# Kernel tuning notes

Hardware: AMD Instinct MI355X
Metric: run time of the kernel (lower is better)

Reference implementation:

```python
import jax, jax.numpy as jnp
import numpy as np

B, NQ, NC1, NC2 = 2, 1024, 1024, 1024
QD = CD1 = CD2 = 1024
H, DH = 8, 64
INNER = H * DH          # 512
VD = 1024               # v_dim, split across heads -> 128 per head
VDH = VD // H


def setup_inputs() -> dict:
    key = jax.random.key(0)
    ks = jax.random.split(key, 18)
    f = lambda k, shape: jax.random.normal(k, shape, jnp.float32) * 0.02
    return {
        "x": f(ks[0], (B, NQ, QD)),
        "context": f(ks[1], (B, NC1, CD1)),
        "context2": f(ks[2], (B, NC2, CD2)),
        "mask1": jax.random.uniform(ks[3], (B, NQ, NC1)) > 0.1,
        "mask2": jax.random.uniform(ks[4], (B, NQ, NC2)) > 0.1,
        "Wq": f(ks[5], (QD, INNER)),  "bq": f(ks[6], (INNER,)),
        "Wk1": f(ks[7], (CD1, INNER)), "bk1": f(ks[8], (INNER,)),
        "Wv1": f(ks[9], (CD1, VD)),    "bv1": f(ks[10], (VD,)),
        "Wk2": f(ks[11], (CD2, INNER)), "bk2": f(ks[12], (INNER,)),
        "Wv2": f(ks[13], (CD2, VD)),    "bv2": f(ks[14], (VD,)),
        "Wo": f(ks[15], (VD, VD)),      "bo": f(ks[16], (VD,)),
    }


def _split_heads(t, d):
    # b n (h d) -> b h n d
    b, n, _ = t.shape
    return t.reshape(b, n, H, d).transpose(0, 2, 1, 3)


def reference(x, context, context2, mask1, mask2,
              Wq, bq, Wk1, bk1, Wv1, bv1, Wk2, bk2, Wv2, bv2, Wo, bo):
    scale = DH ** -0.5
    q = x @ Wq + bq
    k = jnp.concatenate([context @ Wk1 + bk1, context2 @ Wk2 + bk2], axis=1)
    v = jnp.concatenate([context @ Wv1 + bv1, context2 @ Wv2 + bv2], axis=1)

    qh = _split_heads(q, DH)   # [B,H,NQ,DH]
    kh = _split_heads(k, DH)   # [B,H,NC1+NC2,DH]
    vh = _split_heads(v, VDH)  # [B,H,NC1+NC2,VDH]

    sim = jnp.einsum('bhid,bhjd->bhij', qh, kh) * scale  # [B,H,NQ,J]
    mask = jnp.concatenate([mask1, mask2], axis=2)[:, None, :, :]  # [B,1,NQ,J]
    max_neg = -jnp.finfo(sim.dtype).max
    sim = jnp.where(mask, sim, max_neg)

    attn = jax.nn.softmax(sim, axis=-1)
    out = jnp.einsum('bhij,bhjd->bhid', attn, vh)          # [B,H,NQ,VDH]
    out = out.transpose(0, 2, 1, 3).reshape(B, NQ, VD)     # b n (h d)
    return out @ Wo + bo
```

## Files before the change

kernel.cpp:

```cpp
#include <hip/hip_runtime.h>
#include <math.h>

typedef short bf16x8 __attribute__((ext_vector_type(8)));
typedef float f32x4  __attribute__((ext_vector_type(4)));

__device__ __forceinline__ unsigned short f2bf(float f) {
    unsigned int u = __builtin_bit_cast(unsigned int, f);
    u += 0x7FFFu + ((u >> 16) & 1u);
    return (unsigned short)(u >> 16);
}

__device__ __forceinline__ void gld16(const unsigned short* g, unsigned short* l) {
    __builtin_amdgcn_global_load_lds(
        (const __attribute__((address_space(1))) void*)g,
        (__attribute__((address_space(3))) void*)l, 16, 0, 0);
}

__global__ __launch_bounds__(256) void cast3(
    const float* __restrict__ a0, const float* __restrict__ a1, const float* __restrict__ a2,
    unsigned short* __restrict__ o0, unsigned short* __restrict__ o1, unsigned short* __restrict__ o2)
{
    const int z = blockIdx.z;
    const float* a = z == 0 ? a0 : (z == 1 ? a1 : a2);
    unsigned short* o = z == 0 ? o0 : (z == 1 ? o1 : o2);
    size_t i = ((size_t)blockIdx.x * 256 + threadIdx.x) * 8;
    float4 x0 = *(const float4*)&a[i];
    float4 x1 = *(const float4*)&a[i + 4];
    uint4 pk;
    pk.x = (unsigned)f2bf(x0.x) | ((unsigned)f2bf(x0.y) << 16);
    pk.y = (unsigned)f2bf(x0.z) | ((unsigned)f2bf(x0.w) << 16);
    pk.z = (unsigned)f2bf(x1.x) | ((unsigned)f2bf(x1.y) << 16);
    pk.w = (unsigned)f2bf(x1.z) | ((unsigned)f2bf(x1.w) << 16);
    *(uint4*)&o[i] = pk;
}

__global__ __launch_bounds__(256) void cast_t3(
    const float* __restrict__ W0, const float* __restrict__ W1, const float* __restrict__ W2,
    unsigned short* __restrict__ T0, unsigned short* __restrict__ T1, unsigned short* __restrict__ T2,
    int K, int N)
{
    __shared__ float T[64][65];
    const int z = blockIdx.z;
    const float* W = z == 0 ? W0 : (z == 1 ? W1 : W2);
    unsigned short* O = z == 0 ? T0 : (z == 1 ? T1 : T2);
    const int n0 = blockIdx.x << 6, k0 = blockIdx.y << 6;
    const int t = threadIdx.x;
    #pragma unroll
    for (int i = 0; i < 4; i++) {
        int vi = t + (i << 8);
        int r = vi >> 4, c4 = (vi & 15) << 2;
        *(float4*)&T[r][c4] = *(const float4*)&W[(size_t)(k0 + r) * N + n0 + c4];
    }
    __syncthreads();
    #pragma unroll
    for (int i = 0; i < 4; i++) {
        int vi = t + (i << 8);
        int n = vi >> 4, k4 = (vi & 15) << 2;
        uint2 pk;
        pk.x = (unsigned)f2bf(T[k4 + 0][n]) | ((unsigned)f2bf(T[k4 + 1][n]) << 16);
        pk.y = (unsigned)f2bf(T[k4 + 2][n]) | ((unsigned)f2bf(T[k4 + 3][n]) << 16);
        *(uint2*)&O[(size_t)(n0 + n) * K + k0 + k4] = pk;
    }
}

__global__ __launch_bounds__(256) void pack_mask(
    const int* __restrict__ mask1, const int* __restrict__ mask2,
    unsigned long long* __restrict__ mpk)
{
    int wid = (blockIdx.x << 2) + (threadIdx.x >> 6);
    int lane = threadIdx.x & 63;
    const int* m1 = mask1 + ((size_t)wid << 10);
    const int* m2 = mask2 + ((size_t)wid << 10);
    unsigned long long* o = mpk + ((size_t)wid << 5);
    #pragma unroll
    for (int win = 0; win < 16; win++) {
        unsigned long long bal = __ballot(m1[(win << 6) + lane] != 0);
        if (lane == 0) o[win] = bal;
    }
    #pragma unroll
    for (int win = 0; win < 16; win++) {
        unsigned long long bal = __ballot(m2[(win << 6) + lane] != 0);
        if (lane == 0) o[16 + win] = bal;
    }
}

template<int NT>
__device__ __forceinline__ void gemm_core(
    const unsigned short* __restrict__ A,
    const unsigned short* __restrict__ Wt,
    int K, int gm0, int gn0,
    unsigned short (*As)[32], unsigned short (*Bs)[32],
    f32x4 (&acc)[4][NT / 32])
{
    constexpr int NS = NT / 32;
    const int t = threadIdx.x;
    const int lane = t & 63, w = t >> 6;
    const int wm = (w & 1) << 6, wn = (w >> 1) * (NT / 2);
    const int l15 = lane & 15, quad = lane >> 4;

    for (int k0 = 0; k0 < K; k0 += 32) {
        __syncthreads();
        #pragma unroll
        for (int i = 0; i < 2; i++) {
            int r0 = (i << 6) + (w << 4);
            int ra = r0 + (lane >> 2);
            int kc = (lane & 3) << 3;
            gld16(&A[(size_t)(gm0 + ra) * K + k0 + kc], &As[r0][0] + ((size_t)lane << 3));
        }
        #pragma unroll
        for (int i = 0; i < NT / 64; i++) {
            int r0 = (i << 6) + (w << 4);
            int ra = r0 + (lane >> 2);
            int kc = (lane & 3) << 3;
            gld16(&Wt[(size_t)(gn0 + ra) * K + k0 + kc], &Bs[r0][0] + ((size_t)lane << 3));
        }
        __syncthreads();
        bf16x8 af[4], bg[NS];
        #pragma unroll
        for (int i = 0; i < 4; i++)
            af[i] = *(const bf16x8*)&As[wm + (i << 4) + l15][quad << 3];
        #pragma unroll
        for (int j = 0; j < NS; j++)
            bg[j] = *(const bf16x8*)&Bs[wn + (j << 4) + l15][quad << 3];
        #pragma unroll
        for (int i = 0; i < 4; i++)
            #pragma unroll
            for (int j = 0; j < NS; j++)
                acc[i][j] = __builtin_amdgcn_mfma_f32_16x16x32_bf16(af[i], bg[j], acc[i][j], 0, 0, 0);
    }
}

__global__ __launch_bounds__(256) void proj_all(
    const unsigned short* __restrict__ xb, const unsigned short* __restrict__ c1b,
    const unsigned short* __restrict__ c2b,
    const unsigned short* __restrict__ Wqt, const unsigned short* __restrict__ Wk1t,
    const unsigned short* __restrict__ Wk2t, const unsigned short* __restrict__ Wv1t,
    const unsigned short* __restrict__ Wv2t,
    const float* __restrict__ bq, const float* __restrict__ bk1, const float* __restrict__ bk2,
    const float* __restrict__ bv1, const float* __restrict__ bv2,
    unsigned short* __restrict__ qbuf, unsigned short* __restrict__ kbuf,
    unsigned short* __restrict__ vbT)
{
    __shared__ unsigned short As[128][32];
    __shared__ unsigned short Bs[128][32];
    const int bid = blockIdx.x;
    int z, bx, by;
    if (bid < 192) { z = bid >> 6; int l = bid & 63; by = l >> 2; bx = l & 3; }
    else { int l = bid - 192; z = 3 + (l >> 7); l &= 127; by = l >> 3; bx = l & 7; }
    const unsigned short* A  = (z == 0) ? xb : (z == 1 || z == 3) ? c1b : c2b;
    const unsigned short* Wt = (z == 0) ? Wqt : (z == 1) ? Wk1t : (z == 2) ? Wk2t
                             : (z == 3) ? Wv1t : Wv2t;
    const float* bias = (z == 0) ? bq : (z == 1) ? bk1 : (z == 2) ? bk2
                      : (z == 3) ? bv1 : bv2;
    const int gm0 = by << 7, gn0 = bx << 7;

    f32x4 acc[4][4];
    #pragma unroll
    for (int i = 0; i < 4; i++)
        #pragma unroll
        for (int j = 0; j < 4; j++) acc[i][j] = (f32x4){0.f, 0.f, 0.f, 0.f};

    gemm_core<128>(A, Wt, 1024, gm0, gn0, As, Bs, acc);

    const int lane = threadIdx.x & 63, w = threadIdx.x >> 6;
    const int wm = (w & 1) << 6, wn = (w >> 1) << 6;
    const int l15 = lane & 15, quad = lane >> 4;
    float bb[4];
    #pragma unroll
    for (int j = 0; j < 4; j++) bb[j] = bias[gn0 + wn + (j << 4) + l15];

    if (z < 3) {
        unsigned short* out = (z == 0) ? qbuf : kbuf;
        const int obs = (z == 0) ? 1024 : 2048;
        const int off = (z == 2) ? 1024 : 0;
        #pragma unroll
        for (int i = 0; i < 4; i++) {
            int mb = gm0 + wm + (i << 4) + (quad << 2);
            #pragma unroll
            for (int p = 0; p < 4; p++) {
                int m = mb + p;
                int orow = ((m >> 10) * obs) + off + (m & 1023);
                #pragma unroll
                for (int j = 0; j < 4; j++)
                    out[(size_t)orow * 512 + gn0 + wn + (j << 4) + l15] = f2bf(acc[i][j][p] + bb[j]);
            }
        }
    } else {
        const int off = (z == 3) ? 0 : 1024;
        #pragma unroll
        for (int i = 0; i < 4; i++) {
            int mb = gm0 + wm + (i << 4) + (quad << 2);
            int b = mb >> 10;
            int jj = (mb & 1023) + off;
            #pragma unroll
            for (int j = 0; j < 4; j++) {
                int n = gn0 + wn + (j << 4) + l15;
                unsigned long long pk = 0;
                #pragma unroll
                for (int p = 0; p < 4; p++)
                    pk |= (unsigned long long)f2bf(acc[i][j][p] + bb[j]) << (16 * p);
                *(unsigned long long*)&vbT[((size_t)b * 1024 + n) * 2048 + jj] = pk;
            }
        }
    }
}

__global__ __launch_bounds__(256) void gemm_out(
    const unsigned short* __restrict__ abuf, const unsigned short* __restrict__ Wot,
    const float* __restrict__ bo, float* __restrict__ out)
{
    __shared__ unsigned short As[128][32];
    __shared__ unsigned short Bs[64][32];
    const int gm0 = blockIdx.y << 7, gn0 = blockIdx.x << 6;

    f32x4 acc[4][2];
    #pragma unroll
    for (int i = 0; i < 4; i++)
        #pragma unroll
        for (int j = 0; j < 2; j++) acc[i][j] = (f32x4){0.f, 0.f, 0.f, 0.f};

    gemm_core<64>(abuf, Wot, 1024, gm0, gn0, As, Bs, acc);

    const int lane = threadIdx.x & 63, w = threadIdx.x >> 6;
    const int wm = (w & 1) << 6, wn = (w >> 1) << 5;
    const int l15 = lane & 15, quad = lane >> 4;
    float bb[2];
    #pragma unroll
    for (int j = 0; j < 2; j++) bb[j] = bo[gn0 + wn + (j << 4) + l15];
    #pragma unroll
    for (int i = 0; i < 4; i++) {
        int mb = gm0 + wm + (i << 4) + (quad << 2);
        #pragma unroll
        for (int p = 0; p < 4; p++)
            #pragma unroll
            for (int j = 0; j < 2; j++)
                out[(size_t)(mb + p) * 1024 + gn0 + wn + (j << 4) + l15] = acc[i][j][p] + bb[j];
    }
}

__global__ __launch_bounds__(256) void attn_mfma(
    const unsigned short* __restrict__ qbuf, const unsigned short* __restrict__ kbuf,
    const unsigned short* __restrict__ vbT, const unsigned long long* __restrict__ mpk,
    float* __restrict__ Opart, float* __restrict__ ml)
{
    __shared__ unsigned short Ks[128][64];
    __shared__ unsigned short VsT[128][128];
    __shared__ unsigned short Ps[64][132];

    const int t = threadIdx.x;
    const int bid = blockIdx.x;
    const int hs = bid >> 8, r = bid & 255;
    const int h = r & 7, qt = (r >> 3) & 15, b = r >> 7;
    const int q0 = qt << 6;
    const int lane = t & 63, w = t >> 6, l15 = lane & 15, quad = lane >> 4;

    const unsigned short* qrow = qbuf + (((size_t)(b << 10) + q0 + (w << 4) + l15) << 9) + (h << 6);
    const bf16x8 aq0 = *(const bf16x8*)&qrow[quad << 3];
    const bf16x8 aq1 = *(const bf16x8*)&qrow[32 + (quad << 3)];

    f32x4 acc[8];
    #pragma unroll
    for (int ct = 0; ct < 8; ct++) acc[ct] = (f32x4){0.f, 0.f, 0.f, 0.f};
    float m_l = -3.0e38f, l_l = 0.f;

    const size_t kbase = (size_t)b << 20;
    const size_t vbase = ((size_t)((b << 10) + (h << 7))) << 11;
    const unsigned long long* mrow = mpk + (((size_t)(b << 10) + q0 + (w << 4) + l15) << 5);

    for (int jt = 0; jt < 8; jt++) {
        const int j0 = (hs << 10) + (jt << 7);
        __syncthreads();
        #pragma unroll
        for (int i = 0; i < 4; i++) {
            int vi = t + (i << 8);
            int row = vi >> 3, c = vi & 7;
            *(uint4*)&Ks[row][(c ^ (row & 7)) << 3] =
                *(const uint4*)&kbuf[kbase + ((size_t)(j0 + row) << 9) + (h << 6) + (c << 3)];
        }
        #pragma unroll
        for (int i = 0; i < 8; i++) {
            int vi = t + (i << 8);
            int f = vi >> 4, c = vi & 15;
            int sc = (c & 8) | ((c & 7) ^ (f & 7));
            *(uint4*)&VsT[f][sc << 3] =
                *(const uint4*)&vbT[vbase + ((size_t)f << 11) + j0 + (c << 3)];
        }
        __syncthreads();

        f32x4 s[8];
        #pragma unroll
        for (int n = 0; n < 8; n++) {
            int rowk = (n << 4) + l15;
            bf16x8 bk0 = *(const bf16x8*)&Ks[rowk][(quad ^ (l15 & 7)) << 3];
            bf16x8 bk1 = *(const bf16x8*)&Ks[rowk][((quad | 4) ^ (l15 & 7)) << 3];
            s[n] = (f32x4){0.f, 0.f, 0.f, 0.f};
            s[n] = __builtin_amdgcn_mfma_f32_16x16x32_bf16(bk0, aq0, s[n], 0, 0, 0);
            s[n] = __builtin_amdgcn_mfma_f32_16x16x32_bf16(bk1, aq1, s[n], 0, 0, 0);
        }

        const int wbase = j0 >> 6;
        const unsigned long long w0 = mrow[wbase], w1 = mrow[wbase + 1];
        #pragma unroll
        for (int n = 0; n < 8; n++) {
            unsigned long long wd = (n < 4) ? w0 : w1;
            int bit0 = ((n & 3) << 4) + (quad << 2);
            #pragma unroll
            for (int p = 0; p < 4; p++) {
                float sv = s[n][p] * 0.125f;
                s[n][p] = ((wd >> (bit0 + p)) & 1ull) ? sv : -3.0e38f;
            }
        }

        float mt = s[0][0];
        #pragma unroll
        for (int n = 0; n < 8; n++)
            #pragma unroll
            for (int p = 0; p < 4; p++) mt = fmaxf(mt, s[n][p]);
        mt = fmaxf(mt, __shfl_xor(mt, 16, 64));
        mt = fmaxf(mt, __shfl_xor(mt, 32, 64));
        float mn = fmaxf(m_l, mt);
        float ls = 0.f;
        #pragma unroll
        for (int n = 0; n < 8; n++) {
            float e0 = __expf(s[n][0] - mn), e1 = __expf(s[n][1] - mn);
            float e2 = __expf(s[n][2] - mn), e3 = __expf(s[n][3] - mn);
            ls += (e0 + e1) + (e2 + e3);
            unsigned long long pk = (unsigned long long)f2bf(e0)
                | ((unsigned long long)f2bf(e1) << 16)
                | ((unsigned long long)f2bf(e2) << 32)
                | ((unsigned long long)f2bf(e3) << 48);
            *(unsigned long long*)&Ps[(w << 4) + l15][(n << 4) + (quad << 2)] = pk;
        }
        ls += __shfl_xor(ls, 16, 64);
        ls += __shfl_xor(ls, 32, 64);
        float al = __expf(m_l - mn);
        l_l = l_l * al + ls;
        m_l = mn;

        float ar[4];
        #pragma unroll
        for (int p = 0; p < 4; p++)
            ar[p] = __shfl(al, (lane & 48) | ((quad << 2) + p), 64);
        #pragma unroll
        for (int ct = 0; ct < 8; ct++)
            #pragma unroll
            for (int p = 0; p < 4; p++) acc[ct][p] *= ar[p];

        bf16x8 ap[4];
        #pragma unroll
        for (int win = 0; win < 4; win++)
            ap[win] = *(const bf16x8*)&Ps[(w << 4) + l15][(win << 5) + (quad << 3)];
        #pragma unroll
        for (int ct = 0; ct < 8; ct++) {
            int fv = (ct << 4) + l15;
            #pragma unroll
            for (int win = 0; win < 4; win++) {
                int c = (win << 2) + quad;
                int sc = (c & 8) | ((c & 7) ^ (l15 & 7));
                bf16x8 bv = *(const bf16x8*)&VsT[fv][sc << 3];
                acc[ct] = __builtin_amdgcn_mfma_f32_16x16x32_bf16(ap[win], bv, acc[ct], 0, 0, 0);
            }
        }
    }

    #pragma unroll
    for (int p = 0; p < 4; p++) {
        int q = q0 + (w << 4) + (quad << 2) + p;
        size_t idx = (size_t)(hs << 14) + (b << 13) + (h << 10) + q;
        #pragma unroll
        for (int ct = 0; ct < 8; ct++)
            Opart[(idx << 7) + (ct << 4) + l15] = acc[ct][p];
    }
    if (quad == 0) {
        int q = q0 + (w << 4) + l15;
        size_t idx = (size_t)(hs << 14) + (b << 13) + (h << 10) + q;
        ml[(idx << 1) + 0] = m_l;
        ml[(idx << 1) + 1] = l_l;
    }
}

__global__ __launch_bounds__(256) void attn_combine(
    const float* __restrict__ Opart, const float* __restrict__ ml,
    unsigned short* __restrict__ abuf)
{
    int id = (blockIdx.x << 8) + threadIdx.x;
    int bhq = id >> 5, c4 = (id & 31) << 2;
    float2 ml0 = ((const float2*)ml)[bhq];
    float2 ml1 = ((const float2*)ml)[16384 + bhq];
    float M = fmaxf(ml0.x, ml1.x);
    float a0 = __expf(ml0.x - M), a1 = __expf(ml1.x - M);
    float inv = 1.0f / (ml0.y * a0 + ml1.y * a1);
    float4 o0 = *(const float4*)&Opart[((size_t)bhq << 7) + c4];
    float4 o1 = *(const float4*)&Opart[((size_t)(16384 + bhq) << 7) + c4];
    int b = bhq >> 13, hh = (bhq >> 10) & 7, q = bhq & 1023;
    float r0 = (o0.x * a0 + o1.x * a1) * inv;
    float r1 = (o0.y * a0 + o1.y * a1) * inv;
    float r2 = (o0.z * a0 + o1.z * a1) * inv;
    float r3 = (o0.w * a0 + o1.w * a1) * inv;
    unsigned long long pk = (unsigned long long)f2bf(r0)
        | ((unsigned long long)f2bf(r1) << 16)
        | ((unsigned long long)f2bf(r2) << 32)
        | ((unsigned long long)f2bf(r3) << 48);
    *(unsigned long long*)&abuf[((size_t)((b << 10) + q) << 10) + (hh << 7) + c4] = pk;
}

extern "C" void kernel_launch(void* const* d_in, const int* in_sizes, int n_in,
                              void* d_out, int out_size, void* d_ws, size_t ws_size,
                              hipStream_t stream)
{
    const float* x        = (const float*)d_in[0];
    const float* context  = (const float*)d_in[1];
    const float* context2 = (const float*)d_in[2];
    const int*   mask1    = (const int*)d_in[3];
    const int*   mask2    = (const int*)d_in[4];
    const float* Wq  = (const float*)d_in[5];
    const float* bq  = (const float*)d_in[6];
    const float* Wk1 = (const float*)d_in[7];
    const float* bk1 = (const float*)d_in[8];
    const float* Wv1 = (const float*)d_in[9];
    const float* bv1 = (const float*)d_in[10];
    const float* Wk2 = (const float*)d_in[11];
    const float* bk2 = (const float*)d_in[12];
    const float* Wv2 = (const float*)d_in[13];
    const float* bv2 = (const float*)d_in[14];
    const float* Wo  = (const float*)d_in[15];
    const float* bo  = (const float*)d_in[16];
    float* out = (float*)d_out;

    char* W = (char*)d_ws;
    unsigned short* Wot  = (unsigned short*)(W);
    unsigned short* xb   = (unsigned short*)(W + (2ull  << 20));
    unsigned short* c1b  = (unsigned short*)(W + (6ull  << 20));
    unsigned short* c2b  = (unsigned short*)(W + (10ull << 20));
    unsigned short* Wqt  = (unsigned short*)(W + (14ull << 20));
    unsigned short* Wk1t = (unsigned short*)(W + (15ull << 20));
    unsigned short* Wk2t = (unsigned short*)(W + (16ull << 20));
    unsigned short* Wv1t = (unsigned short*)(W + (17ull << 20));
    unsigned short* Wv2t = (unsigned short*)(W + (19ull << 20));
    unsigned short* qbuf = (unsigned short*)(W + (21ull << 20));
    unsigned short* kbuf = (unsigned short*)(W + (23ull << 20));
    unsigned short* vbT  = (unsigned short*)(W + (27ull << 20));
    float*              Opart = (float*)(W + (2ull << 20));
    unsigned long long* mpk   = (unsigned long long*)(W + (18ull << 20));
    float*              mlb   = (float*)(W + (18ull << 20) + (1ull << 19));
    unsigned short*     abuf  = (unsigned short*)(W + (19ull << 20));

    cast3   <<<dim3(1024, 1, 3), 256, 0, stream>>>(x, context, context2, xb, c1b, c2b);
    cast_t3 <<<dim3(8, 16, 3),   256, 0, stream>>>(Wq, Wk1, Wk2, Wqt, Wk1t, Wk2t, 1024, 512);
    cast_t3 <<<dim3(16, 16, 3),  256, 0, stream>>>(Wv1, Wv2, Wo, Wv1t, Wv2t, Wot, 1024, 1024);
    proj_all<<<dim3(448),        256, 0, stream>>>(xb, c1b, c2b, Wqt, Wk1t, Wk2t, Wv1t, Wv2t,
                                                   bq, bk1, bk2, bv1, bv2, qbuf, kbuf, vbT);
    pack_mask<<<dim3(512),       256, 0, stream>>>(mask1, mask2, mpk);
    attn_mfma<<<dim3(512),       256, 0, stream>>>(qbuf, kbuf, vbT, mpk, Opart, mlb);
    attn_combine<<<dim3(2048),   256, 0, stream>>>(Opart, mlb, abuf);
    gemm_out<<<dim3(16, 16),     256, 0, stream>>>(abuf, Wot, bo, out);
}
```

Measured before the change: 240.2 us.

## Fuse prep kernels, head-major swizzled K/V, 4-way split attention with bf16 partials

```diff
diff --git a/kernel.cpp b/kernel.cpp
--- a/kernel.cpp
+++ b/kernel.cpp
@@ -9,6 +9,9 @@
     u += 0x7FFFu + ((u >> 16) & 1u);
     return (unsigned short)(u >> 16);
 }
+__device__ __forceinline__ float bf2f(unsigned short u) {
+    return __builtin_bit_cast(float, (unsigned int)u << 16);
+}
 
 __device__ __forceinline__ void gld16(const unsigned short* g, unsigned short* l) {
     __builtin_amdgcn_global_load_lds(
@@ -16,71 +19,91 @@
         (__attribute__((address_space(3))) void*)l, 16, 0, 0);
 }
 
-__global__ __launch_bounds__(256) void cast3(
-    const float* __restrict__ a0, const float* __restrict__ a1, const float* __restrict__ a2,
-    unsigned short* __restrict__ o0, unsigned short* __restrict__ o1, unsigned short* __restrict__ o2)
-{
-    const int z = blockIdx.z;
-    const float* a = z == 0 ? a0 : (z == 1 ? a1 : a2);
-    unsigned short* o = z == 0 ? o0 : (z == 1 ? o1 : o2);
-    size_t i = ((size_t)blockIdx.x * 256 + threadIdx.x) * 8;
-    float4 x0 = *(const float4*)&a[i];
-    float4 x1 = *(const float4*)&a[i + 4];
-    uint4 pk;
-    pk.x = (unsigned)f2bf(x0.x) | ((unsigned)f2bf(x0.y) << 16);
-    pk.y = (unsigned)f2bf(x0.z) | ((unsigned)f2bf(x0.w) << 16);
-    pk.z = (unsigned)f2bf(x1.x) | ((unsigned)f2bf(x1.y) << 16);
-    pk.w = (unsigned)f2bf(x1.z) | ((unsigned)f2bf(x1.w) << 16);
-    *(uint4*)&o[i] = pk;
-}
-
-__global__ __launch_bounds__(256) void cast_t3(
-    const float* __restrict__ W0, const float* __restrict__ W1, const float* __restrict__ W2,
-    unsigned short* __restrict__ T0, unsigned short* __restrict__ T1, unsigned short* __restrict__ T2,
-    int K, int N)
+__global__ __launch_bounds__(256) void prep(
+    const float* __restrict__ x, const float* __restrict__ c1, const float* __restrict__ c2,
+    const int* __restrict__ mask1, const int* __restrict__ mask2,
+    const float* __restrict__ Wq, const float* __restrict__ Wk1, const float* __restrict__ Wk2,
+    const float* __restrict__ Wv1, const float* __restrict__ Wv2, const float* __restrict__ Wo,
+    unsigned short* __restrict__ xb, unsigned short* __restrict__ c1b, unsigned short* __restrict__ c2b,
+    unsigned short* __restrict__ Wqt, unsigned short* __restrict__ Wk1t, unsigned short* __restrict__ Wk2t,
+    unsigned short* __restrict__ Wv1t, unsigned short* __restrict__ Wv2t, unsigned short* __restrict__ Wot,
+    unsigned long long* __restrict__ mpk)
 {
     __shared__ float T[64][65];
-    const int z = blockIdx.z;
-    const float* W = z == 0 ? W0 : (z == 1 ? W1 : W2);
-    unsigned short* O = z == 0 ? T0 : (z == 1 ? T1 : T2);
-    const int n0 = blockIdx.x << 6, k0 = blockIdx.y << 6;
-    const int t = threadIdx.x;
-    #pragma unroll
-    for (int i = 0; i < 4; i++) {
-        int vi = t + (i << 8);
-        int r = vi >> 4, c4 = (vi & 15) << 2;
-        *(float4*)&T[r][c4] = *(const float4*)&W[(size_t)(k0 + r) * N + n0 + c4];
-    }
-    __syncthreads();
-    #pragma unroll
-    for (int i = 0; i < 4; i++) {
-        int vi = t + (i << 8);
-        int n = vi >> 4, k4 = (vi & 15) << 2;
-        uint2 pk;
-        pk.x = (unsigned)f2bf(T[k4 + 0][n]) | ((unsigned)f2bf(T[k4 + 1][n]) << 16);
-        pk.y = (unsigned)f2bf(T[k4 + 2][n]) | ((unsigned)f2bf(T[k4 + 3][n]) << 16);
-        *(uint2*)&O[(size_t)(n0 + n) * K + k0 + k4] = pk;
-    }
-}
-
-__global__ __launch_bounds__(256) void pack_mask(
-    const int* __restrict__ mask1, const int* __restrict__ mask2,
-    unsigned long long* __restrict__ mpk)
-{
-    int wid = (blockIdx.x << 2) + (threadIdx.x >> 6);
-    int lane = threadIdx.x & 63;
-    const int* m1 = mask1 + ((size_t)wid << 10);
-    const int* m2 = mask2 + ((size_t)wid << 10);
-    unsigned long long* o = mpk + ((size_t)wid << 5);
-    #pragma unroll
-    for (int win = 0; win < 16; win++) {
-        unsigned long long bal = __ballot(m1[(win << 6) + lane] != 0);
-        if (lane == 0) o[win] = bal;
-    }
-    #pragma unroll
-    for (int win = 0; win < 16; win++) {
-        unsigned long long bal = __ballot(m2[(win << 6) + lane] != 0);
-        if (lane == 0) o[16 + win] = bal;
+    const int bid = blockIdx.x, t = threadIdx.x;
+
+    if (bid < 3072) {
+        const int z = bid >> 10;
+        const float* a = z == 0 ? x : (z == 1 ? c1 : c2);
+        unsigned short* o = z == 0 ? xb : (z == 1 ? c1b : c2b);
+        size_t i = ((size_t)(bid & 1023) * 256 + t) * 8;
+        float4 x0 = *(const float4*)&a[i];
+        float4 x1 = *(const float4*)&a[i + 4];
+        uint4 pk;
+        pk.x = (unsigned)f2bf(x0.x) | ((unsigned)f2bf(x0.y) << 16);
+        pk.y = (unsigned)f2bf(x0.z) | ((unsigned)f2bf(x0.w) << 16);
+        pk.z = (unsigned)f2bf(x1.x) | ((unsigned)f2bf(x1.y) << 16);
+        pk.w = (unsigned)f2bf(x1.z) | ((unsigned)f2bf(x1.w) << 16);
+        *(uint4*)&o[i] = pk;
+        return;
+    }
+    if (bid < 4224) {
+        const float* W; unsigned short* O; int N, n0, k0; bool perm = false;
+        if (bid < 3456) {
+            int l = bid - 3072, z = l >> 7, rem = l & 127;
+            W = z == 0 ? Wq : (z == 1 ? Wk1 : Wk2);
+            O = z == 0 ? Wqt : (z == 1 ? Wk1t : Wk2t);
+            N = 512; n0 = (rem & 7) << 6; k0 = (rem >> 3) << 6;
+        } else {
+            int l = bid - 3456, z = l >> 8, rem = l & 255;
+            W = z == 0 ? Wv1 : (z == 1 ? Wv2 : Wo);
+            O = z == 0 ? Wv1t : (z == 1 ? Wv2t : Wot);
+            N = 1024; n0 = (rem & 15) << 6; k0 = (rem >> 4) << 6;
+            perm = (z == 2);
+        }
+        #pragma unroll
+        for (int i = 0; i < 4; i++) {
+            int vi = t + (i << 8);
+            int r = vi >> 4, c4 = (vi & 15) << 2;
+            *(float4*)&T[r][c4] = *(const float4*)&W[(size_t)(k0 + r) * N + n0 + c4];
+        }
+        __syncthreads();
+        #pragma unroll
+        for (int i = 0; i < 4; i++) {
+            int vi = t + (i << 8);
+            int n = vi >> 4, k4 = (vi & 15) << 2;
+            if (!perm) {
+                uint2 pk;
+                pk.x = (unsigned)f2bf(T[k4 + 0][n]) | ((unsigned)f2bf(T[k4 + 1][n]) << 16);
+                pk.y = (unsigned)f2bf(T[k4 + 2][n]) | ((unsigned)f2bf(T[k4 + 3][n]) << 16);
+                *(uint2*)&O[(size_t)(n0 + n) * 1024 + k0 + k4] = pk;
+            } else {
+                #pragma unroll
+                for (int ii = 0; ii < 4; ii++) {
+                    int k = k0 + k4 + ii, f = k & 127;
+                    int kp = (k & ~127) | ((f & 15) << 3) | (f >> 4);
+                    O[(size_t)(n0 + n) * 1024 + kp] = f2bf(T[k4 + ii][n]);
+                }
+            }
+        }
+        return;
+    }
+    {
+        int wid = ((bid - 4224) << 2) + (t >> 6);
+        int lane = t & 63;
+        const int* m1 = mask1 + ((size_t)wid << 10);
+        const int* m2 = mask2 + ((size_t)wid << 10);
+        unsigned long long* o = mpk + ((size_t)wid << 5);
+        #pragma unroll
+        for (int win = 0; win < 16; win++) {
+            unsigned long long bal = __ballot(m1[(win << 6) + lane] != 0);
+            if (lane == 0) o[win] = bal;
+        }
+        #pragma unroll
+        for (int win = 0; win < 16; win++) {
+            unsigned long long bal = __ballot(m2[(win << 6) + lane] != 0);
+            if (lane == 0) o[16 + win] = bal;
+        }
     }
 }
 
@@ -138,8 +161,8 @@
     const unsigned short* __restrict__ Wv2t,
     const float* __restrict__ bq, const float* __restrict__ bk1, const float* __restrict__ bk2,
     const float* __restrict__ bv1, const float* __restrict__ bv2,
-    unsigned short* __restrict__ qbuf, unsigned short* __restrict__ kbuf,
-    unsigned short* __restrict__ vbT)
+    unsigned short* __restrict__ qbuf, unsigned short* __restrict__ khb,
+    unsigned short* __restrict__ vhb)
 {
     __shared__ unsigned short As[128][32];
     __shared__ unsigned short Bs[128][32];
@@ -169,20 +192,33 @@
     #pragma unroll
     for (int j = 0; j < 4; j++) bb[j] = bias[gn0 + wn + (j << 4) + l15];
 
-    if (z < 3) {
-        unsigned short* out = (z == 0) ? qbuf : kbuf;
-        const int obs = (z == 0) ? 1024 : 2048;
-        const int off = (z == 2) ? 1024 : 0;
+    if (z == 0) {
         #pragma unroll
         for (int i = 0; i < 4; i++) {
             int mb = gm0 + wm + (i << 4) + (quad << 2);
             #pragma unroll
-            for (int p = 0; p < 4; p++) {
-                int m = mb + p;
-                int orow = ((m >> 10) * obs) + off + (m & 1023);
+            for (int p = 0; p < 4; p++)
                 #pragma unroll
                 for (int j = 0; j < 4; j++)
-                    out[(size_t)orow * 512 + gn0 + wn + (j << 4) + l15] = f2bf(acc[i][j][p] + bb[j]);
+                    qbuf[(size_t)(mb + p) * 512 + gn0 + wn + (j << 4) + l15] = f2bf(acc[i][j][p] + bb[j]);
+        }
+    } else if (z < 3) {
+        const int off = (z == 2) ? 1024 : 0;
+        #pragma unroll
+        for (int i = 0; i < 4; i++) {
+            int mb = gm0 + wm + (i << 4) + (quad << 2);
+            int b = mb >> 10;
+            #pragma unroll
+            for (int j = 0; j < 4; j++) {
+                int n = gn0 + wn + (j << 4) + l15;
+                int hh = n >> 6, d = n & 63;
+                size_t hb = ((size_t)((b << 3) + hh) << 17);
+                #pragma unroll
+                for (int p = 0; p < 4; p++) {
+                    int jrow = off + ((mb + p) & 1023);
+                    khb[hb + ((size_t)jrow << 6) + ((((d >> 3) ^ (jrow & 7))) << 3) + (d & 7)]
+                        = f2bf(acc[i][j][p] + bb[j]);
+                }
             }
         }
     } else {
@@ -195,11 +231,14 @@
             #pragma unroll
             for (int j = 0; j < 4; j++) {
                 int n = gn0 + wn + (j << 4) + l15;
+                int hh = n >> 7, f = n & 127;
+                size_t base = ((size_t)((b << 3) + hh) << 18) + ((size_t)f << 11);
+                int jpos = (jj & ~63) | ((((jj >> 3) & 7) ^ (f & 7)) << 3) | (jj & 7);
                 unsigned long long pk = 0;
                 #pragma unroll
                 for (int p = 0; p < 4; p++)
                     pk |= (unsigned long long)f2bf(acc[i][j][p] + bb[j]) << (16 * p);
-                *(unsigned long long*)&vbT[((size_t)b * 1024 + n) * 2048 + jj] = pk;
+                *(unsigned long long*)&vhb[base + jpos] = pk;
             }
         }
     }
@@ -239,13 +278,13 @@
 }
 
 __global__ __launch_bounds__(256) void attn_mfma(
-    const unsigned short* __restrict__ qbuf, const unsigned short* __restrict__ kbuf,
-    const unsigned short* __restrict__ vbT, const unsigned long long* __restrict__ mpk,
-    float* __restrict__ Opart, float* __restrict__ ml)
-{
-    __shared__ unsigned short Ks[128][64];
-    __shared__ unsigned short VsT[128][128];
-    __shared__ unsigned short Ps[64][132];
+    const unsigned short* __restrict__ qbuf, const unsigned short* __restrict__ khb,
+    const unsigned short* __restrict__ vhb, const unsigned long long* __restrict__ mpk,
+    unsigned short* __restrict__ Opart, float* __restrict__ ml)
+{
+    __shared__ unsigned short Ks[64 * 64];
+    __shared__ unsigned short VsT[128 * 64];
+    __shared__ unsigned short Ps[64 * 64];
 
     const int t = threadIdx.x;
     const int bid = blockIdx.x;
@@ -253,6 +292,7 @@
     const int h = r & 7, qt = (r >> 3) & 15, b = r >> 7;
     const int q0 = qt << 6;
     const int lane = t & 63, w = t >> 6, l15 = lane & 15, quad = lane >> 4;
+    const int v7 = l15 & 7;
 
     const unsigned short* qrow = qbuf + (((size_t)(b << 10) + q0 + (w << 4) + l15) << 9) + (h << 6);
     const bf16x8 aq0 = *(const bf16x8*)&qrow[quad << 3];
@@ -263,57 +303,51 @@
     for (int ct = 0; ct < 8; ct++) acc[ct] = (f32x4){0.f, 0.f, 0.f, 0.f};
     float m_l = -3.0e38f, l_l = 0.f;
 
-    const size_t kbase = (size_t)b << 20;
-    const size_t vbase = ((size_t)((b << 10) + (h << 7))) << 11;
-    const unsigned long long* mrow = mpk + (((size_t)(b << 10) + q0 + (w << 4) + l15) << 5);
+    const unsigned short* kh = khb + ((size_t)((b << 3) + h) << 17);
+    const unsigned short* vh = vhb + ((size_t)((b << 3) + h) << 18);
+    const unsigned long long* mrow = mpk + (((size_t)(b << 10) + q0 + (w << 4) + l15) << 5) + (hs << 3);
+    const int prow = ((w << 4) + l15) << 6;
 
     for (int jt = 0; jt < 8; jt++) {
-        const int j0 = (hs << 10) + (jt << 7);
+        const int j0 = (hs << 9) + (jt << 6);
         __syncthreads();
-        #pragma unroll
-        for (int i = 0; i < 4; i++) {
-            int vi = t + (i << 8);
-            int row = vi >> 3, c = vi & 7;
-            *(uint4*)&Ks[row][(c ^ (row & 7)) << 3] =
-                *(const uint4*)&kbuf[kbase + ((size_t)(j0 + row) << 9) + (h << 6) + (c << 3)];
-        }
-        #pragma unroll
-        for (int i = 0; i < 8; i++) {
-            int vi = t + (i << 8);
-            int f = vi >> 4, c = vi & 15;
-            int sc = (c & 8) | ((c & 7) ^ (f & 7));
-            *(uint4*)&VsT[f][sc << 3] =
-                *(const uint4*)&vbT[vbase + ((size_t)f << 11) + j0 + (c << 3)];
+        {
+            const unsigned short* kg = kh + ((size_t)j0 << 6);
+            int o = (w << 10) + (lane << 3);
+            gld16(kg + o, Ks + o);
+            gld16(kg + o + 512, Ks + o + 512);
+        }
+        #pragma unroll
+        for (int it = 0; it < 4; it++) {
+            int f0 = (w << 5) + (it << 3);
+            gld16(vh + ((size_t)(f0 + (lane >> 3)) << 11) + j0 + ((lane & 7) << 3),
+                  VsT + (f0 << 6) + (lane << 3));
         }
         __syncthreads();
 
-        f32x4 s[8];
-        #pragma unroll
-        for (int n = 0; n < 8; n++) {
+        const unsigned long long mw = mrow[jt];
+
+        f32x4 s[4];
+        #pragma unroll
+        for (int n = 0; n < 4; n++) {
             int rowk = (n << 4) + l15;
-            bf16x8 bk0 = *(const bf16x8*)&Ks[rowk][(quad ^ (l15 & 7)) << 3];
-            bf16x8 bk1 = *(const bf16x8*)&Ks[rowk][((quad | 4) ^ (l15 & 7)) << 3];
+            bf16x8 bk0 = *(const bf16x8*)&Ks[(rowk << 6) + ((quad ^ v7) << 3)];
+            bf16x8 bk1 = *(const bf16x8*)&Ks[(rowk << 6) + (((quad + 4) ^ v7) << 3)];
             s[n] = (f32x4){0.f, 0.f, 0.f, 0.f};
             s[n] = __builtin_amdgcn_mfma_f32_16x16x32_bf16(bk0, aq0, s[n], 0, 0, 0);
             s[n] = __builtin_amdgcn_mfma_f32_16x16x32_bf16(bk1, aq1, s[n], 0, 0, 0);
         }
-
-        const int wbase = j0 >> 6;
-        const unsigned long long w0 = mrow[wbase], w1 = mrow[wbase + 1];
-        #pragma unroll
-        for (int n = 0; n < 8; n++) {
-            unsigned long long wd = (n < 4) ? w0 : w1;
-            int bit0 = ((n & 3) << 4) + (quad << 2);
+        #pragma unroll
+        for (int n = 0; n < 4; n++)
             #pragma unroll
             for (int p = 0; p < 4; p++) {
                 float sv = s[n][p] * 0.125f;
-                s[n][p] = ((wd >> (bit0 + p)) & 1ull) ? sv : -3.0e38f;
+                s[n][p] = ((mw >> ((n << 4) + (quad << 2) + p)) & 1ull) ? sv : -3.0e38f;
             }
-        }
 
         float mt = s[0][0];
         #pragma unroll
-        for (int n = 0; n < 8; n++)
+        for (int n = 0; n < 4; n++)
             #pragma unroll
             for (int p = 0; p < 4; p++) mt = fmaxf(mt, s[n][p]);
         mt = fmaxf(mt, __shfl_xor(mt, 16, 64));
@@ -321,7 +355,7 @@
         float mn = fmaxf(m_l, mt);
         float ls = 0.f;
         #pragma unroll
-        for (int n = 0; n < 8; n++) {
+        for (int n = 0; n < 4; n++) {
             float e0 = __expf(s[n][0] - mn), e1 = __expf(s[n][1] - mn);
             float e2 = __expf(s[n][2] - mn), e3 = __expf(s[n][3] - mn);
             ls += (e0 + e1) + (e2 + e3);
@@ -329,7 +363,8 @@
                 | ((unsigned long long)f2bf(e1) << 16)
                 | ((unsigned long long)f2bf(e2) << 32)
                 | ((unsigned long long)f2bf(e3) << 48);
-            *(unsigned long long*)&Ps[(w << 4) + l15][(n << 4) + (quad << 2)] = pk;
+            int mblk = ((n << 1) + (quad >> 1)) ^ v7;
+            *(unsigned long long*)&Ps[prow + (mblk << 3) + ((quad & 1) << 2)] = pk;
         }
         ls += __shfl_xor(ls, 16, 64);
         ls += __shfl_xor(ls, 32, 64);
@@ -346,18 +381,19 @@
             #pragma unroll
             for (int p = 0; p < 4; p++) acc[ct][p] *= ar[p];
 
-        bf16x8 ap[4];
-        #pragma unroll
-        for (int win = 0; win < 4; win++)
-            ap[win] = *(const bf16x8*)&Ps[(w << 4) + l15][(win << 5) + (quad << 3)];
+        bf16x8 ap[2];
+        #pragma unroll
+        for (int win = 0; win < 2; win++) {
+            int mblk = ((win << 2) + quad) ^ v7;
+            ap[win] = *(const bf16x8*)&Ps[prow + (mblk << 3)];
+        }
         #pragma unroll
         for (int ct = 0; ct < 8; ct++) {
-            int fv = (ct << 4) + l15;
-            #pragma unroll
-            for (int win = 0; win < 4; win++) {
+            int f = (ct << 4) + l15;
+            #pragma unroll
+            for (int win = 0; win < 2; win++) {
                 int c = (win << 2) + quad;
-                int sc = (c & 8) | ((c & 7) ^ (l15 & 7));
-                bf16x8 bv = *(const bf16x8*)&VsT[fv][sc << 3];
+                bf16x8 bv = *(const bf16x8*)&VsT[(f << 6) + ((c ^ v7) << 3)];
                 acc[ct] = __builtin_amdgcn_mfma_f32_16x16x32_bf16(ap[win], bv, acc[ct], 0, 0, 0);
             }
         }
@@ -366,42 +402,53 @@
     #pragma unroll
     for (int p = 0; p < 4; p++) {
         int q = q0 + (w << 4) + (quad << 2) + p;
-        size_t idx = (size_t)(hs << 14) + (b << 13) + (h << 10) + q;
-        #pragma unroll
-        for (int ct = 0; ct < 8; ct++)
-            Opart[(idx << 7) + (ct << 4) + l15] = acc[ct][p];
+        size_t idx = ((size_t)hs << 14) + ((size_t)((b << 3) + h) << 10) + q;
+        uint4 pk;
+        pk.x = (unsigned)f2bf(acc[0][p]) | ((unsigned)f2bf(acc[1][p]) << 16);
+        pk.y = (unsigned)f2bf(acc[2][p]) | ((unsigned)f2bf(acc[3][p]) << 16);
+        pk.z = (unsigned)f2bf(acc[4][p]) | ((unsigned)f2bf(acc[5][p]) << 16);
+        pk.w = (unsigned)f2bf(acc[6][p]) | ((unsigned)f2bf(acc[7][p]) << 16);
+        *(uint4*)&Opart[(idx << 7) + (l15 << 3)] = pk;
     }
     if (quad == 0) {
         int q = q0 + (w << 4) + l15;
-        size_t idx = (size_t)(hs << 14) + (b << 13) + (h << 10) + q;
+        size_t idx = ((size_t)hs << 14) + ((size_t)((b << 3) + h) << 10) + q;
         ml[(idx << 1) + 0] = m_l;
         ml[(idx << 1) + 1] = l_l;
     }
 }
 
 __global__ __launch_bounds__(256) void attn_combine(
-    const float* __restrict__ Opart, const float* __restrict__ ml,
+    const unsigned short* __restrict__ Opart, const float* __restrict__ ml,
     unsigned short* __restrict__ abuf)
 {
     int id = (blockIdx.x << 8) + threadIdx.x;
-    int bhq = id >> 5, c4 = (id & 31) << 2;
-    float2 ml0 = ((const float2*)ml)[bhq];
-    float2 ml1 = ((const float2*)ml)[16384 + bhq];
-    float M = fmaxf(ml0.x, ml1.x);
-    float a0 = __expf(ml0.x - M), a1 = __expf(ml1.x - M);
-    float inv = 1.0f / (ml0.y * a0 + ml1.y * a1);
-    float4 o0 = *(const float4*)&Opart[((size_t)bhq << 7) + c4];
-    float4 o1 = *(const float4*)&Opart[((size_t)(16384 + bhq) << 7) + c4];
+    int bhq = id >> 5, c = id & 31;
+    float2 m0 = ((const float2*)ml)[bhq];
+    float2 m1 = ((const float2*)ml)[16384 + bhq];
+    float2 m2 = ((const float2*)ml)[32768 + bhq];
+    float2 m3 = ((const float2*)ml)[49152 + bhq];
+    float M = fmaxf(fmaxf(m0.x, m1.x), fmaxf(m2.x, m3.x));
+    float a0 = __expf(m0.x - M), a1 = __expf(m1.x - M);
+    float a2 = __expf(m2.x - M), a3 = __expf(m3.x - M);
+    float inv = 1.0f / (m0.y * a0 + m1.y * a1 + m2.y * a2 + m3.y * a3);
+    a0 *= inv; a1 *= inv; a2 *= inv; a3 *= inv;
+    float o[4] = {0.f, 0.f, 0.f, 0.f};
+    float as[4] = {a0, a1, a2, a3};
+    #pragma unroll
+    for (int s = 0; s < 4; s++) {
+        uint2 v = *(const uint2*)&Opart[((size_t)(s * 16384 + bhq) << 7) + (c << 2)];
+        o[0] += as[s] * bf2f((unsigned short)(v.x & 0xFFFF));
+        o[1] += as[s] * bf2f((unsigned short)(v.x >> 16));
+        o[2] += as[s] * bf2f((unsigned short)(v.y & 0xFFFF));
+        o[3] += as[s] * bf2f((unsigned short)(v.y >> 16));
+    }
     int b = bhq >> 13, hh = (bhq >> 10) & 7, q = bhq & 1023;
-    float r0 = (o0.x * a0 + o1.x * a1) * inv;
-    float r1 = (o0.y * a0 + o1.y * a1) * inv;
-    float r2 = (o0.z * a0 + o1.z * a1) * inv;
-    float r3 = (o0.w * a0 + o1.w * a1) * inv;
-    unsigned long long pk = (unsigned long long)f2bf(r0)
-        | ((unsigned long long)f2bf(r1) << 16)
-        | ((unsigned long long)f2bf(r2) << 32)
-        | ((unsigned long long)f2bf(r3) << 48);
-    *(unsigned long long*)&abuf[((size_t)((b << 10) + q) << 10) + (hh << 7) + c4] = pk;
+    unsigned long long pk = (unsigned long long)f2bf(o[0])
+        | ((unsigned long long)f2bf(o[1]) << 16)
+        | ((unsigned long long)f2bf(o[2]) << 32)
+        | ((unsigned long long)f2bf(o[3]) << 48);
+    *(unsigned long long*)&abuf[((size_t)((b << 10) + q) << 10) + (hh << 7) + (c << 2)] = pk;
 }
 
 extern "C" void kernel_launch(void* const* d_in, const int* in_sizes, int n_in,
@@ -438,20 +485,19 @@
     unsigned short* Wv1t = (unsigned short*)(W + (17ull << 20));
     unsigned short* Wv2t = (unsigned short*)(W + (19ull << 20));
     unsigned short* qbuf = (unsigned short*)(W + (21ull << 20));
-    unsigned short* kbuf = (unsigned short*)(W + (23ull << 20));
-    unsigned short* vbT  = (unsigned short*)(W + (27ull << 20));
-    float*              Opart = (float*)(W + (2ull << 20));
-    unsigned long long* mpk   = (unsigned long long*)(W + (18ull << 20));
-    float*              mlb   = (float*)(W + (18ull << 20) + (1ull << 19));
-    unsigned short*     abuf  = (unsigned short*)(W + (19ull << 20));
-
-    cast3   <<<dim3(1024, 1, 3), 256, 0, stream>>>(x, context, context2, xb, c1b, c2b);
-    cast_t3 <<<dim3(8, 16, 3),   256, 0, stream>>>(Wq, Wk1, Wk2, Wqt, Wk1t, Wk2t, 1024, 512);
-    cast_t3 <<<dim3(16, 16, 3),  256, 0, stream>>>(Wv1, Wv2, Wo, Wv1t, Wv2t, Wot, 1024, 1024);
-    proj_all<<<dim3(448),        256, 0, stream>>>(xb, c1b, c2b, Wqt, Wk1t, Wk2t, Wv1t, Wv2t,
-                                                   bq, bk1, bk2, bv1, bv2, qbuf, kbuf, vbT);
-    pack_mask<<<dim3(512),       256, 0, stream>>>(mask1, mask2, mpk);
-    attn_mfma<<<dim3(512),       256, 0, stream>>>(qbuf, kbuf, vbT, mpk, Opart, mlb);
-    attn_combine<<<dim3(2048),   256, 0, stream>>>(Opart, mlb, abuf);
-    gemm_out<<<dim3(16, 16),     256, 0, stream>>>(abuf, Wot, bo, out);
-}
+    unsigned short* khb  = (unsigned short*)(W + (23ull << 20));
+    unsigned short* vhb  = (unsigned short*)(W + (27ull << 20));
+    unsigned long long* mpk = (unsigned long long*)(W + (35ull << 20));
+    float*          mlb  = (float*)(W + (35ull << 20) + (1ull << 19));
+    unsigned short* Opart = (unsigned short*)(W + (2ull << 20));
+    unsigned short* abuf  = (unsigned short*)(W + (19ull << 20));
+
+    prep<<<dim3(4736), 256, 0, stream>>>(x, context, context2, mask1, mask2,
+                                         Wq, Wk1, Wk2, Wv1, Wv2, Wo,
+                                         xb, c1b, c2b, Wqt, Wk1t, Wk2t, Wv1t, Wv2t, Wot, mpk);
+    proj_all<<<dim3(448), 256, 0, stream>>>(xb, c1b, c2b, Wqt, Wk1t, Wk2t, Wv1t, Wv2t,
+                                            bq, bk1, bk2, bv1, bv2, qbuf, khb, vhb);
+    attn_mfma<<<dim3(1024), 256, 0, stream>>>(qbuf, khb, vhb, mpk, Opart, mlb);
+    attn_combine<<<dim3(2048), 256, 0, stream>>>(Opart, mlb, abuf);
+    gemm_out<<<dim3(16, 16), 256, 0, stream>>>(abuf, Wot, bo, out);
+}
```

Result: faster. 218.0 us (-9.2%).
